# Kernel optimization log

Measured on AMD Instinct MI355X. Metric: run time of the kernel, lower is better.

## Reference

```python
import jax, jax.numpy as jnp
import numpy as np


def floor_ste(x):
    # forward: floor(x); backward: identity (straight-through estimator)
    return x + jax.lax.stop_gradient(jnp.floor(x) - x)


def _int_polynomial(x_int, sf):
    c0, c1, c2 = 0.35815147, 0.96963238, 1.0
    b_int = floor_ste((c1 / c0) / sf)
    c_int = floor_ste((c2 / c0) / (sf * sf))
    z = x_int * (x_int + b_int) + c_int
    return z, c0 * sf * sf


def _int_exp(x_int, sf):
    x0 = -0.69314718
    n = 15
    x0_int = floor_ste(x0 / sf)
    x_int = jnp.maximum(x_int, n * x0_int)
    q = floor_ste(x_int / x0_int)
    r = x_int - x0_int * q
    exp_int, exp_sf = _int_polynomial(r, sf)
    exp_int = jnp.maximum(floor_ste(exp_int * jnp.exp2(n - q)), 0.0)
    return exp_int, exp_sf / (2.0 ** n)


def _int_softmax(x, sf):
    x_int = x / sf
    x_int = x_int - jnp.max(x_int, axis=-1, keepdims=True)
    exp_int, exp_sf = _int_exp(x_int, sf)
    exp_int_sum = jnp.sum(exp_int, axis=-1, keepdims=True)
    return exp_int, exp_int_sum, exp_sf


def setup_inputs() -> dict:
    key = jax.random.key(0)
    k1, = jax.random.split(key, 1)
    x = jax.random.normal(k1, (2, 16, 1024, 1024), dtype=jnp.float32)
    scale = jnp.float32(0.05)          # activation quantization step
    threshold = jnp.array([0.1], dtype=jnp.float32)  # nn.Parameter init
    return {"x": x, "scale": scale, "threshold": threshold}


def reference(x, scale, threshold):
    output_bit = 8
    threshold_bits = 8
    exp_int, exp_int_sum, exp_sf = _int_softmax(x, scale)
    factor = floor_ste((2.0 ** 32) / exp_int_sum)
    out_scale_A = threshold / (2.0 ** output_bit - 1.0)   # shape [1]
    out_scale_B = 1.0 / (2.0 ** output_bit - 1.0)
    approx_threshold = (floor_ste(threshold * 2.0 ** threshold_bits)
                        * exp_int_sum / (2.0 ** threshold_bits))
    mask_A = exp_int <= approx_threshold
    exp_int_A = jnp.where(mask_A, exp_int, 0.0)
    exp_int_B = jnp.where(mask_A, 0.0, exp_int)
    softmax_int_A = floor_ste(exp_int_A * factor / ((2.0 ** 32) * out_scale_A))
    softmax_int_B = floor_ste(exp_int_B * factor / ((2.0 ** 32) * out_scale_B))
    softmax_int_B = jnp.minimum(softmax_int_B, 255.0)
    return softmax_int_A * out_scale_A + softmax_int_B * out_scale_B
```

## Files before the change

### kernel.cpp

```cpp
#include <hip/hip_runtime.h>
#include <math.h>

#pragma clang fp contract(off)

#define TPB 256
#define ROWLEN 1024

typedef float f32x4 __attribute__((ext_vector_type(4)));


__device__ __forceinline__ float wave_max_dpp(float m) {
    const int NEG_INF = 0xff800000;
    int v;
    v = __builtin_amdgcn_update_dpp(NEG_INF, __float_as_int(m), 0x111, 0xf, 0xf, false);
    m = fmaxf(m, __int_as_float(v));
    v = __builtin_amdgcn_update_dpp(NEG_INF, __float_as_int(m), 0x112, 0xf, 0xf, false);
    m = fmaxf(m, __int_as_float(v));
    v = __builtin_amdgcn_update_dpp(NEG_INF, __float_as_int(m), 0x114, 0xf, 0xf, false);
    m = fmaxf(m, __int_as_float(v));
    v = __builtin_amdgcn_update_dpp(NEG_INF, __float_as_int(m), 0x118, 0xf, 0xf, false);
    m = fmaxf(m, __int_as_float(v));
    v = __builtin_amdgcn_update_dpp(NEG_INF, __float_as_int(m), 0x142, 0xa, 0xf, false);
    m = fmaxf(m, __int_as_float(v));
    v = __builtin_amdgcn_update_dpp(NEG_INF, __float_as_int(m), 0x143, 0xc, 0xf, false);
    m = fmaxf(m, __int_as_float(v));
    return __int_as_float(__builtin_amdgcn_readlane(__float_as_int(m), 63));
}

__device__ __forceinline__ unsigned wave_sum_dpp_u32(unsigned a) {
    int v;
    v = __builtin_amdgcn_update_dpp(0, (int)a, 0x111, 0xf, 0xf, false); a += (unsigned)v;
    v = __builtin_amdgcn_update_dpp(0, (int)a, 0x112, 0xf, 0xf, false); a += (unsigned)v;
    v = __builtin_amdgcn_update_dpp(0, (int)a, 0x114, 0xf, 0xf, false); a += (unsigned)v;
    v = __builtin_amdgcn_update_dpp(0, (int)a, 0x118, 0xf, 0xf, false); a += (unsigned)v;
    v = __builtin_amdgcn_update_dpp(0, (int)a, 0x142, 0xa, 0xf, false); a += (unsigned)v;
    v = __builtin_amdgcn_update_dpp(0, (int)a, 0x143, 0xc, 0xf, false); a += (unsigned)v;
    return (unsigned)__builtin_amdgcn_readlane((int)a, 63);
}

__global__ __launch_bounds__(TPB) void qsplit_int_softmax_kernel(
    const float* __restrict__ x,
    const float* __restrict__ scale_p,
    const float* __restrict__ thr_p,
    float* __restrict__ out)
{
    const int lane = threadIdx.x & 63;
    const int wid  = threadIdx.x >> 6;
    const int row  = blockIdx.x * 4 + wid;
    const size_t rbase = (size_t)row * ROWLEN + (size_t)lane * 4;

    const float sf  = scale_p[0];
    const float thr = thr_p[0];

    const double sfd  = (double)sf;
    const double rd   = 1.0 / sfd;
    const float  rh   = (float)rd;
    const float  rl   = (float)(rd - (double)rh);

    const double x0d    = floor(-0.69314718 / sfd);
    const float  x0f    = (float)x0d;
    const float  bfc    = (float)floor((0.96963238 / 0.35815147) / sfd);
    const float  cfc    = (float)floor((1.0 / 0.35815147) / (sfd * sfd));
    const float  clampf = (float)(15.0 * x0d);
    const float  invx0f = (float)(1.0 / x0d);

    const float  osA  = thr / 255.0f;
    const float  osB  = 1.0f / 255.0f;
    const float  invA = (float)(1.0 / (4294967296.0 * (double)osA));
    const float  invB = (float)(1.0 / (4294967296.0 * (double)osB));
    const double thrq = floor((double)thr * 256.0);

    f32x4 xv[4];
    #pragma unroll
    for (int k = 0; k < 4; ++k)
        xv[k] = *(const f32x4*)(x + rbase + (size_t)k * 256);

    float xi[16];
    #pragma unroll
    for (int k = 0; k < 4; ++k) {
        #pragma unroll
        for (int jj = 0; jj < 4; ++jj) {
            const float xx = xv[k][jj];
            const float p  = xx * rh;
            const float e  = __builtin_fmaf(xx, rh, -p);
            xi[k*4+jj]     = p + __builtin_fmaf(xx, rl, e);
        }
    }

    float m = xi[0];
    #pragma unroll
    for (int j = 1; j < 16; ++j) m = fmaxf(m, xi[j]);
    m = wave_max_dpp(m);

    float e16[16];
    unsigned int usum = 0;
    #pragma unroll
    for (int j = 0; j < 16; ++j) {
        float v = xi[j] - m;
        v = fmaxf(v, clampf);
        const float qf = floorf(v * invx0f);
        const int   qi = (int)qf;
        const float r2 = v - x0f * qf;
        const float t  = r2 + bfc;
        const float z  = r2 * t + cfc;
        float ei = floorf(ldexpf(z, 15 - qi));
        ei = fmaxf(ei, 0.0f);
        e16[j] = ei;
        usum += (unsigned int)ei;
    }

    const unsigned lo = wave_sum_dpp_u32(usum & 0xFFFFu);
    const unsigned hi = wave_sum_dpp_u32(usum >> 16);
    const unsigned long long ws = ((unsigned long long)hi << 16) + lo;
    const double s = (double)ws;

    const double factor_d = floor(4294967296.0 / s);
    const float  fac_f = (float)factor_d;
    const float  ath_f = (float)((thrq * s) * (1.0 / 256.0));

    #pragma unroll
    for (int k = 0; k < 4; ++k) {
        f32x4 o;
        #pragma unroll
        for (int jj = 0; jj < 4; ++jj) {
            const float ei  = e16[k*4+jj];
            const bool  isA = (ei <= ath_f);
            const float t1  = ei * fac_f;
            const float t2  = t1 * (isA ? invA : invB);
            float si = floorf(t2);
            si = fminf(si, isA ? 3.0e38f : 255.0f);
            o[jj] = si * (isA ? osA : osB);
        }
        __builtin_nontemporal_store(o, (f32x4*)(out + rbase + (size_t)k * 256));
    }
}

extern "C" void kernel_launch(void* const* d_in, const int* in_sizes, int n_in,
                              void* d_out, int out_size, void* d_ws, size_t ws_size,
                              hipStream_t stream) {
    const float* x     = (const float*)d_in[0];
    const float* scale = (const float*)d_in[1];
    const float* thr   = (const float*)d_in[2];
    float* out = (float*)d_out;

    const int total = in_sizes[0];
    const int rows  = total / ROWLEN;
    const int blocks = rows / 4;

    qsplit_int_softmax_kernel<<<dim3(blocks), dim3(TPB), 0, stream>>>(
        x, scale, thr, out);
}
```

Before: 231.5 us.

## Process one row per block with cross-wave LDS reductions, float setup math

Each block of 256 threads now handles a single 1024-element row with 4 elements per thread, instead of one row per wave with 16 elements per lane. Row max and row sum are combined across the four waves through shared memory and two __syncthreads. The per-thread constant setup switches from double to float, using a double-float reciprocal trick to keep precision. The aim is fewer registers and higher occupancy, at the cost of block-level barriers and four times as many blocks.

```diff
diff --git a/kernel.cpp b/kernel.cpp
--- a/kernel.cpp
+++ b/kernel.cpp
@@ -7,7 +7,6 @@
 #define ROWLEN 1024
 
 typedef float f32x4 __attribute__((ext_vector_type(4)));
-
 
 __device__ __forceinline__ float wave_max_dpp(float m) {
     const int NEG_INF = 0xff800000;
@@ -44,95 +43,98 @@
     const float* __restrict__ thr_p,
     float* __restrict__ out)
 {
-    const int lane = threadIdx.x & 63;
-    const int wid  = threadIdx.x >> 6;
-    const int row  = blockIdx.x * 4 + wid;
-    const size_t rbase = (size_t)row * ROWLEN + (size_t)lane * 4;
+    const int tid  = threadIdx.x;
+    const int lane = tid & 63;
+    const int wid  = tid >> 6;
+    const size_t base = (size_t)blockIdx.x * ROWLEN + (size_t)tid * 4;
+
+    __shared__ float  smax[4];
+    __shared__ double ssum[4];
 
     const float sf  = scale_p[0];
     const float thr = thr_p[0];
 
-    const double sfd  = (double)sf;
-    const double rd   = 1.0 / sfd;
-    const float  rh   = (float)rd;
-    const float  rl   = (float)(rd - (double)rh);
+    const float rh = 1.0f / sf;
+    const float er = __builtin_fmaf(-sf, rh, 1.0f);
+    const float rl = rh * er;
 
-    const double x0d    = floor(-0.69314718 / sfd);
-    const float  x0f    = (float)x0d;
-    const float  bfc    = (float)floor((0.96963238 / 0.35815147) / sfd);
-    const float  cfc    = (float)floor((1.0 / 0.35815147) / (sfd * sfd));
-    const float  clampf = (float)(15.0 * x0d);
-    const float  invx0f = (float)(1.0 / x0d);
+    #define DF_DIV(a) ({ float _p = (a) * rh; \
+                         float _e = __builtin_fmaf((a), rh, -_p); \
+                         _p + __builtin_fmaf((a), rl, _e); })
+    const float x0f    = floorf(DF_DIV(-0.69314718f));
+    const float bfc    = floorf(DF_DIV(2.7073824f));
+    const float s2     = sf * sf;
+    const float r2h    = 1.0f / s2;
+    const float r2e    = __builtin_fmaf(-s2, r2h, 1.0f);
+    const float r2l    = r2h * r2e;
+    const float cq     = __builtin_fmaf(2.7921141f, r2l,
+                         2.7921141f * r2h);
+    const float cfc    = floorf(cq);
+    const float clampf = 15.0f * x0f;
+    const float invx0f = 1.0f / x0f;
 
-    const float  osA  = thr / 255.0f;
-    const float  osB  = 1.0f / 255.0f;
-    const float  invA = (float)(1.0 / (4294967296.0 * (double)osA));
-    const float  invB = (float)(1.0 / (4294967296.0 * (double)osB));
-    const double thrq = floor((double)thr * 256.0);
+    const float osA  = thr / 255.0f;
+    const float osB  = 1.0f / 255.0f;
+    const float invA = 1.0f / (4294967296.0f * osA);
+    const float invB = 1.0f / (4294967296.0f * osB);
+    const float thrq = floorf(thr * 256.0f);
 
-    f32x4 xv[4];
+    const f32x4 xv = *(const f32x4*)(x + base);
+
+    float xi[4];
     #pragma unroll
-    for (int k = 0; k < 4; ++k)
-        xv[k] = *(const f32x4*)(x + rbase + (size_t)k * 256);
-
-    float xi[16];
-    #pragma unroll
-    for (int k = 0; k < 4; ++k) {
-        #pragma unroll
-        for (int jj = 0; jj < 4; ++jj) {
-            const float xx = xv[k][jj];
-            const float p  = xx * rh;
-            const float e  = __builtin_fmaf(xx, rh, -p);
-            xi[k*4+jj]     = p + __builtin_fmaf(xx, rl, e);
-        }
+    for (int j = 0; j < 4; ++j) {
+        const float xx = xv[j];
+        const float p  = xx * rh;
+        const float e  = __builtin_fmaf(xx, rh, -p);
+        xi[j] = p + __builtin_fmaf(xx, rl, e);
     }
 
-    float m = xi[0];
+    float m = fmaxf(fmaxf(xi[0], xi[1]), fmaxf(xi[2], xi[3]));
+    m = wave_max_dpp(m);
+    if (lane == 0) smax[wid] = m;
+    __syncthreads();
+    m = fmaxf(fmaxf(smax[0], smax[1]), fmaxf(smax[2], smax[3]));
+
+    float e4[4];
+    unsigned usum = 0;
     #pragma unroll
-    for (int j = 1; j < 16; ++j) m = fmaxf(m, xi[j]);
-    m = wave_max_dpp(m);
-
-    float e16[16];
-    unsigned int usum = 0;
-    #pragma unroll
-    for (int j = 0; j < 16; ++j) {
+    for (int j = 0; j < 4; ++j) {
         float v = xi[j] - m;
         v = fmaxf(v, clampf);
         const float qf = floorf(v * invx0f);
         const int   qi = (int)qf;
-        const float r2 = v - x0f * qf;
-        const float t  = r2 + bfc;
-        const float z  = r2 * t + cfc;
+        const float r  = v - x0f * qf;
+        const float t  = r + bfc;
+        const float z  = r * t + cfc;
         float ei = floorf(ldexpf(z, 15 - qi));
         ei = fmaxf(ei, 0.0f);
-        e16[j] = ei;
-        usum += (unsigned int)ei;
+        e4[j] = ei;
+        usum += (unsigned)ei;
     }
 
     const unsigned lo = wave_sum_dpp_u32(usum & 0xFFFFu);
     const unsigned hi = wave_sum_dpp_u32(usum >> 16);
-    const unsigned long long ws = ((unsigned long long)hi << 16) + lo;
-    const double s = (double)ws;
+    if (lane == 0)
+        ssum[wid] = (double)(((unsigned long long)hi << 16) + lo);
+    __syncthreads();
+    const double s = ((ssum[0] + ssum[1]) + ssum[2]) + ssum[3];
 
-    const double factor_d = floor(4294967296.0 / s);
-    const float  fac_f = (float)factor_d;
-    const float  ath_f = (float)((thrq * s) * (1.0 / 256.0));
+    const float fac_f = (float)floor(4294967296.0 / s);
+    const float ath_f = (float)(((double)thrq * s) * (1.0 / 256.0));
 
+    f32x4 o;
     #pragma unroll
-    for (int k = 0; k < 4; ++k) {
-        f32x4 o;
-        #pragma unroll
-        for (int jj = 0; jj < 4; ++jj) {
-            const float ei  = e16[k*4+jj];
-            const bool  isA = (ei <= ath_f);
-            const float t1  = ei * fac_f;
-            const float t2  = t1 * (isA ? invA : invB);
-            float si = floorf(t2);
-            si = fminf(si, isA ? 3.0e38f : 255.0f);
-            o[jj] = si * (isA ? osA : osB);
-        }
-        __builtin_nontemporal_store(o, (f32x4*)(out + rbase + (size_t)k * 256));
+    for (int j = 0; j < 4; ++j) {
+        const float ei  = e4[j];
+        const bool  isA = (ei <= ath_f);
+        const float t1  = ei * fac_f;
+        const float t2  = t1 * (isA ? invA : invB);
+        float si = floorf(t2);
+        si = fminf(si, isA ? 3.0e38f : 255.0f);
+        o[j] = si * (isA ? osA : osB);
     }
+    __builtin_nontemporal_store(o, (f32x4*)(out + base));
 }
 
 extern "C" void kernel_launch(void* const* d_in, const int* in_sizes, int n_in,
@@ -145,8 +147,7 @@
 
     const int total = in_sizes[0];
     const int rows  = total / ROWLEN;
-    const int blocks = rows / 4;
 
-    qsplit_int_softmax_kernel<<<dim3(blocks), dim3(TPB), 0, stream>>>(
+    qsplit_int_softmax_kernel<<<dim3(rows), dim3(TPB), 0, stream>>>(
         x, scale, thr, out);
 }
```

After: 224.4 us. -3.1%, faster.
